# Optimization experiments

Measured on AMD Instinct MI355X. Metric: run time of the kernel, lower is better.

Reference implementation:

```python
import jax, jax.numpy as jnp
import numpy as np

TEMPERATURE = 0.07
BASE_TEMPERATURE = 0.07
EPS = 1e-10


def setup_inputs() -> dict:
    key = jax.random.key(0)
    k1, k2, k3 = jax.random.split(key, 3)
    bsz, n_views, d = 4096, 2, 256
    features = jax.random.normal(k1, (bsz, n_views, d), dtype=jnp.float32)
    # L2-normalize views as is standard for SupCon inputs (keeps logits sane)
    features = features / jnp.linalg.norm(features, axis=-1, keepdims=True)
    va_labels = jax.random.normal(k2, (bsz, 2), dtype=jnp.float32)
    batch_belong_diaID = jax.random.randint(k3, (bsz,), 0, 512, dtype=jnp.int64)
    return {
        "features": features,
        "va_labels": va_labels,
        "batch_belong_diaID": batch_belong_diaID,
        "thres_dict": 1,
    }


def reference(features, va_labels, batch_belong_diaID, thres_dict):
    bsz, n_views, d = features.shape
    dtype = features.dtype

    # --- vectorized mask construction (replaces O(bsz^2) python loops) ---
    eye = jnp.eye(bsz, dtype=bool)
    same_dia = batch_belong_diaID[:, None] == batch_belong_diaID[None, :]
    diff = va_labels[:, None, :] - va_labels[None, :, :]          # [bsz, bsz, 2]
    euclid = jnp.sqrt(jnp.sum(diff * diff, axis=-1))              # [bsz, bsz]
    close_va = euclid < thres_dict
    # final mask: diagonal | same dialogue | VA-close (off-diag terms; diag already 1)
    mask = (eye | same_dia | close_va).astype(dtype)
    mask = jax.lax.stop_gradient(mask)  # mask build is non-differentiable in torch too

    # --- contrastive loss (contrast_mode='one') ---
    # torch.cat(torch.unbind(features, 1), 0): view-major stacking
    contrast_feature = features.transpose(1, 0, 2).reshape(n_views * bsz, d)
    anchor_feature = features[:, 0]                               # anchor_count = 1

    logits = jnp.matmul(anchor_feature, contrast_feature.T) / TEMPERATURE  # [bsz, n_views*bsz]
    logits = logits - jax.lax.stop_gradient(jnp.max(logits, axis=1, keepdims=True))

    mask_t = jnp.tile(mask, (1, n_views))                          # [bsz, n_views*bsz]
    # logits_mask: zero out self-contrast (column i for anchor row i)
    idx = jnp.arange(bsz)
    logits_mask = jnp.ones((bsz, n_views * bsz), dtype=dtype).at[idx, idx].set(0.0)
    mask_t = mask_t * logits_mask

    exp_logits = jnp.exp(logits) * logits_mask
    log_prob = logits - jnp.log(jnp.sum(exp_logits, axis=1, keepdims=True) + EPS)

    mean_log_prob_pos = jnp.sum(mask_t * log_prob, axis=1) / (jnp.sum(mask_t, axis=1) + EPS)
    loss = jnp.mean(-mean_log_prob_pos)  # anchor_count=1 -> plain mean over bsz
    return loss
```

## Files before the change

### kernel.cpp

```cpp
#include <hip/hip_runtime.h>
#include <hip/hip_bf16.h>

#define BSZ   4096
#define NCON  8192
#define DFEAT 256
#define C2    20.60992914f
#define LN2   0.6931471806f

#define BJM 16
#define BI 128
#define NJT 8
#define JSTRIP_M (NJT * BJM)

typedef __attribute__((ext_vector_type(8))) short short8;
typedef __attribute__((ext_vector_type(4))) float f32x4;

__device__ __forceinline__ unsigned short f2bf(float f) {
    __hip_bfloat16 h = __float2bfloat16(f);
    return *reinterpret_cast<unsigned short*>(&h);
}

__device__ __forceinline__ void gload_lds16(const void* g, void* l) {
    __builtin_amdgcn_global_load_lds(
        (const __attribute__((address_space(1))) unsigned int*)g,
        (__attribute__((address_space(3))) unsigned int*)l,
        16, 0, 0);
}

__device__ __forceinline__ void gload_reg16(const void* p, short8& dst) {
    unsigned long long a = (unsigned long long)p;
    asm volatile("global_load_dwordx4 %0, %1, off"
                 : "=v"(dst) : "v"(a));
}


__global__ __launch_bounds__(256) void k_prep(const float* __restrict__ feat,
                                              unsigned short* __restrict__ con,
                                              float* __restrict__ acc) {
    int idx = blockIdx.x * 256 + threadIdx.x;
    int e = idx * 4;
    int j = e >> 8;
    int k = e & 255;
    int src = (j < BSZ) ? ((j * 2) * DFEAT + k)
                        : (((j - BSZ) * 2 + 1) * DFEAT + k);
    float4 f = *(const float4*)(feat + src);
    ushort4 o;
    o.x = f2bf(f.x); o.y = f2bf(f.y); o.z = f2bf(f.z); o.w = f2bf(f.w);
    *(ushort4*)(con + e) = o;
    if (idx < 3 * BSZ) acc[idx] = 0.0f;
}

__global__ __launch_bounds__(256) void k_main(const __hip_bfloat16* __restrict__ conp,
                                              const float* __restrict__ va,
                                              const int* __restrict__ dia,
                                              const int* __restrict__ thr_ptr,
                                              float* __restrict__ Srow,
                                              float* __restrict__ Arow,
                                              float* __restrict__ Brow) {
    __shared__ short lX[2][2][BJM * DFEAT];
    __shared__ float s_vjx[JSTRIP_M], s_vjy[JSTRIP_M];
    __shared__ int   s_dj[JSTRIP_M];

    const int tid  = threadIdx.x;
    const int lane = tid & 63;
    const int wv   = tid >> 6;
    const int l15  = lane & 15;
    const int hi   = lane >> 4;
    const int jmbase = blockIdx.x * JSTRIP_M;
    const int ibase  = blockIdx.y * BI + wv * 32;
    const short* cs = (const short*)conp;

    auto stageX = [&](int buf, int jt) {
        #pragma unroll
        for (int v = 0; v < 2; ++v) {
            #pragma unroll
            for (int q = 0; q < 2; ++q) {
                int e   = q * 2048 + tid * 8;
                int col = e & 63;
                int row = (e >> 6) & 15;
                int k2  = e >> 10;
                int scol = col ^ ((row & 7) << 3);
                gload_lds16(cs + (size_t)(jmbase + jt * BJM + row + v * BSZ) * DFEAT
                               + k2 * 64 + scol,
                            &lX[buf][v][e]);
            }
        }
    };

    stageX(0, 0);

    const short* yrow0 = cs + (size_t)(ibase + l15) * DFEAT + hi * 8;
    short8 y[2][8];
    #pragma unroll
    for (int n = 0; n < 2; ++n)
        #pragma unroll
        for (int s = 0; s < 8; ++s)
            gload_reg16(yrow0 + (size_t)n * 16 * DFEAT + s * 32, y[n][s]);

    if (tid < JSTRIP_M) {
        int jm = jmbase + tid;
        s_vjx[tid] = va[2 * jm]; s_vjy[tid] = va[2 * jm + 1]; s_dj[tid] = dia[jm];
    }

    int raw = *thr_ptr;
    float t_ = (raw > 0 && raw < 100000) ? (float)raw : __int_as_float(raw);
    float thres2 = t_ * t_;

    float vix[2], viy[2]; int di[2], ig[2];
    #pragma unroll
    for (int n = 0; n < 2; ++n) {
        ig[n] = ibase + n * 16 + l15;
        vix[n] = va[2 * ig[n]]; viy[n] = va[2 * ig[n] + 1]; di[n] = dia[ig[n]];
    }

    float sp[2] = {0.f, 0.f};
    float ap[2] = {0.f, 0.f};
    float bp[2] = {0.f, 0.f};

    __syncthreads();
    asm volatile("s_waitcnt vmcnt(0)" ::: "memory");
    __builtin_amdgcn_sched_barrier(0);

    for (int jt = 0; jt < NJT; ++jt) {
        const int cur = jt & 1;
        if (jt < NJT - 1) stageX(cur ^ 1, jt + 1);

        f32x4 acc[2][2];
        #pragma unroll
        for (int v = 0; v < 2; ++v)
            #pragma unroll
            for (int n = 0; n < 2; ++n)
                acc[v][n] = (f32x4){0.f, 0.f, 0.f, 0.f};

        __builtin_amdgcn_s_setprio(1);
        #pragma unroll
        for (int s = 0; s < 8; ++s) {
            const int base = (s >> 1) * 2048;
            const int colb = (s & 1) * 64 + hi * 16;
            const int row  = l15;
            const int off  = base + row * 128 + (colb ^ ((row & 7) << 4));
            short8 x0 = *(const short8*)((const char*)&lX[cur][0][0] + off);
            short8 x1 = *(const short8*)((const char*)&lX[cur][1][0] + off);
            #pragma unroll
            for (int n = 0; n < 2; ++n) {
                acc[0][n] = __builtin_amdgcn_mfma_f32_16x16x32_bf16(x0, y[n][s], acc[0][n], 0, 0, 0);
                acc[1][n] = __builtin_amdgcn_mfma_f32_16x16x32_bf16(x1, y[n][s], acc[1][n], 0, 0, 0);
            }
        }
        __builtin_amdgcn_s_setprio(0);

        const int jt0 = jt * BJM;
        #pragma unroll
        for (int r = 0; r < 4; ++r) {
            const int jl  = jt0 + hi * 4 + r;
            const int jmg = jmbase + jl;
            float vjx = s_vjx[jl], vjy = s_vjy[jl];
            int dj = s_dj[jl];
            #pragma unroll
            for (int n = 0; n < 2; ++n) {
                float l0 = __builtin_fmaf(acc[0][n][r], C2, -C2);
                float l1 = __builtin_fmaf(acc[1][n][r], C2, -C2);
                float dx = vix[n] - vjx, dy = viy[n] - vjy;
                bool diag = (ig[n] == jmg);
                bool mk = (di[n] == dj) | (dx * dx + dy * dy < thres2);
                float e0 = diag ? 0.0f : exp2f(l0);
                float e1 = exp2f(l1);
                sp[n] += e0 + e1;
                float mm = mk ? 1.0f : 0.0f;
                ap[n] = __builtin_fmaf(mm, l0 + l1, ap[n]);
                bp[n] += mm;
            }
        }
        __syncthreads();
    }

    #pragma unroll
    for (int n = 0; n < 2; ++n) {
        float s = sp[n], a = ap[n], b = bp[n];
        s += __shfl_xor(s, 16, 64);  a += __shfl_xor(a, 16, 64);  b += __shfl_xor(b, 16, 64);
        s += __shfl_xor(s, 32, 64);  a += __shfl_xor(a, 32, 64);  b += __shfl_xor(b, 32, 64);
        if (hi == 0) {
            atomicAdd(&Srow[ig[n]], s);
            atomicAdd(&Arow[ig[n]], a * LN2);
            atomicAdd(&Brow[ig[n]], b);
        }
    }
}

__global__ __launch_bounds__(256) void k_final(const float* __restrict__ S,
                                               const float* __restrict__ A,
                                               const float* __restrict__ B,
                                               float* __restrict__ out) {
    __shared__ float red[256];
    float sum = 0.f;
    for (int i = threadIdx.x; i < BSZ; i += 256) {
        float b = 2.0f * B[i] - 1.0f;
        float v = (A[i] - b * logf(S[i] + 1e-10f)) / (b + 1e-10f);
        sum += -v;
    }
    red[threadIdx.x] = sum;
    __syncthreads();
    for (int s = 128; s > 0; s >>= 1) {
        if (threadIdx.x < s) red[threadIdx.x] += red[threadIdx.x + s];
        __syncthreads();
    }
    if (threadIdx.x == 0) out[0] = red[0] / (float)BSZ;
}

extern "C" void kernel_launch(void* const* d_in, const int* in_sizes, int n_in,
                              void* d_out, int out_size, void* d_ws, size_t ws_size,
                              hipStream_t stream) {
    const float* feat = (const float*)d_in[0];
    const float* va   = (const float*)d_in[1];
    const int*   dia  = (const int*)d_in[2];
    const int*   thr  = (const int*)d_in[3];

    unsigned short* con = (unsigned short*)d_ws;
    float* acc = (float*)((char*)d_ws + (size_t)NCON * DFEAT * 2);
    float* out = (float*)d_out;

    k_prep<<<(NCON * DFEAT / 4 + 255) / 256, 256, 0, stream>>>(feat, con, acc);

    dim3 grid(BSZ / JSTRIP_M, BSZ / BI);
    k_main<<<grid, 256, 0, stream>>>((const __hip_bfloat16*)con, va, dia, thr,
                                     acc, acc + BSZ, acc + 2 * BSZ);

    k_final<<<1, 256, 0, stream>>>(acc, acc + BSZ, acc + 2 * BSZ, out);
}
```

Measured before the change: 51.06 us.

## Double j-tile height to 32 rows with precomputed staging pointers and packed metadata

Doubles the per-iteration j tile from 16 to 32 rows, so each wave now runs 8 MFMAs per k-step over two 16-row sub-tiles and each strip covers 256 columns. This halves the grid's x dimension and the number of barriers per unit of work. Global-to-LDS staging addresses are now precomputed once and advanced by pointer increments. Per-column va/dialog metadata is packed into one float4 LDS array so it needs a single load. The trade-off is twice the LDS for the double buffer, about 64KB, which may lower occupancy, plus more accumulator registers and fewer blocks in flight.

```diff
diff --git a/kernel.cpp b/kernel.cpp
--- a/kernel.cpp
+++ b/kernel.cpp
@@ -7,7 +7,7 @@
 #define C2    20.60992914f
 #define LN2   0.6931471806f
 
-#define BJM 16
+#define BJM 32
 #define BI 128
 #define NJT 8
 #define JSTRIP_M (NJT * BJM)
@@ -58,8 +58,7 @@
                                               float* __restrict__ Arow,
                                               float* __restrict__ Brow) {
     __shared__ short lX[2][2][BJM * DFEAT];
-    __shared__ float s_vjx[JSTRIP_M], s_vjy[JSTRIP_M];
-    __shared__ int   s_dj[JSTRIP_M];
+    __shared__ float4 s_meta[JSTRIP_M];
 
     const int tid  = threadIdx.x;
     const int lane = tid & 63;
@@ -70,24 +69,30 @@
     const int ibase  = blockIdx.y * BI + wv * 32;
     const short* cs = (const short*)conp;
 
-    auto stageX = [&](int buf, int jt) {
-        #pragma unroll
-        for (int v = 0; v < 2; ++v) {
-            #pragma unroll
-            for (int q = 0; q < 2; ++q) {
-                int e   = q * 2048 + tid * 8;
-                int col = e & 63;
-                int row = (e >> 6) & 15;
-                int k2  = e >> 10;
-                int scol = col ^ ((row & 7) << 3);
-                gload_lds16(cs + (size_t)(jmbase + jt * BJM + row + v * BSZ) * DFEAT
-                               + k2 * 64 + scol,
-                            &lX[buf][v][e]);
+    const short* pg[2][4];
+    #pragma unroll
+    for (int v = 0; v < 2; ++v)
+        #pragma unroll
+        for (int q = 0; q < 4; ++q) {
+            int e   = q * 2048 + tid * 8;
+            int col = e & 63;
+            int row = (e >> 6) & 31;
+            int k2  = e >> 11;
+            int scol = col ^ ((row & 7) << 3);
+            pg[v][q] = cs + (size_t)(jmbase + row + v * BSZ) * DFEAT + k2 * 64 + scol;
+        }
+
+    auto stageX = [&](int buf) {
+        #pragma unroll
+        for (int v = 0; v < 2; ++v)
+            #pragma unroll
+            for (int q = 0; q < 4; ++q) {
+                gload_lds16(pg[v][q], &lX[buf][v][q * 2048 + tid * 8]);
+                pg[v][q] += BJM * DFEAT;
             }
-        }
     };
 
-    stageX(0, 0);
+    stageX(0);
 
     const short* yrow0 = cs + (size_t)(ibase + l15) * DFEAT + hi * 8;
     short8 y[2][8];
@@ -97,9 +102,10 @@
         for (int s = 0; s < 8; ++s)
             gload_reg16(yrow0 + (size_t)n * 16 * DFEAT + s * 32, y[n][s]);
 
-    if (tid < JSTRIP_M) {
+    {
         int jm = jmbase + tid;
-        s_vjx[tid] = va[2 * jm]; s_vjy[tid] = va[2 * jm + 1]; s_dj[tid] = dia[jm];
+        s_meta[tid] = make_float4(va[2 * jm], va[2 * jm + 1],
+                                  __int_as_float(dia[jm]), 0.0f);
     }
 
     int raw = *thr_ptr;
@@ -123,54 +129,66 @@
 
     for (int jt = 0; jt < NJT; ++jt) {
         const int cur = jt & 1;
-        if (jt < NJT - 1) stageX(cur ^ 1, jt + 1);
-
-        f32x4 acc[2][2];
+        if (jt < NJT - 1) stageX(cur ^ 1);
+
+        f32x4 acc[2][2][2];
         #pragma unroll
         for (int v = 0; v < 2; ++v)
             #pragma unroll
-            for (int n = 0; n < 2; ++n)
-                acc[v][n] = (f32x4){0.f, 0.f, 0.f, 0.f};
+            for (int m = 0; m < 2; ++m)
+                #pragma unroll
+                for (int n = 0; n < 2; ++n)
+                    acc[v][m][n] = (f32x4){0.f, 0.f, 0.f, 0.f};
 
         __builtin_amdgcn_s_setprio(1);
         #pragma unroll
         for (int s = 0; s < 8; ++s) {
-            const int base = (s >> 1) * 2048;
+            const int base = (s >> 1) * 4096;
             const int colb = (s & 1) * 64 + hi * 16;
-            const int row  = l15;
-            const int off  = base + row * 128 + (colb ^ ((row & 7) << 4));
-            short8 x0 = *(const short8*)((const char*)&lX[cur][0][0] + off);
-            short8 x1 = *(const short8*)((const char*)&lX[cur][1][0] + off);
-            #pragma unroll
-            for (int n = 0; n < 2; ++n) {
-                acc[0][n] = __builtin_amdgcn_mfma_f32_16x16x32_bf16(x0, y[n][s], acc[0][n], 0, 0, 0);
-                acc[1][n] = __builtin_amdgcn_mfma_f32_16x16x32_bf16(x1, y[n][s], acc[1][n], 0, 0, 0);
-            }
+            short8 xf[2][2];
+            #pragma unroll
+            for (int v = 0; v < 2; ++v)
+                #pragma unroll
+                for (int m = 0; m < 2; ++m) {
+                    int row = m * 16 + l15;
+                    xf[v][m] = *(const short8*)((const char*)&lX[cur][v][0]
+                                 + base + row * 128 + (colb ^ ((row & 7) << 4)));
+                }
+            #pragma unroll
+            for (int v = 0; v < 2; ++v)
+                #pragma unroll
+                for (int m = 0; m < 2; ++m)
+                    #pragma unroll
+                    for (int n = 0; n < 2; ++n)
+                        acc[v][m][n] = __builtin_amdgcn_mfma_f32_16x16x32_bf16(
+                            xf[v][m], y[n][s], acc[v][m][n], 0, 0, 0);
         }
         __builtin_amdgcn_s_setprio(0);
 
         const int jt0 = jt * BJM;
         #pragma unroll
-        for (int r = 0; r < 4; ++r) {
-            const int jl  = jt0 + hi * 4 + r;
-            const int jmg = jmbase + jl;
-            float vjx = s_vjx[jl], vjy = s_vjy[jl];
-            int dj = s_dj[jl];
-            #pragma unroll
-            for (int n = 0; n < 2; ++n) {
-                float l0 = __builtin_fmaf(acc[0][n][r], C2, -C2);
-                float l1 = __builtin_fmaf(acc[1][n][r], C2, -C2);
-                float dx = vix[n] - vjx, dy = viy[n] - vjy;
-                bool diag = (ig[n] == jmg);
-                bool mk = (di[n] == dj) | (dx * dx + dy * dy < thres2);
-                float e0 = diag ? 0.0f : exp2f(l0);
-                float e1 = exp2f(l1);
-                sp[n] += e0 + e1;
-                float mm = mk ? 1.0f : 0.0f;
-                ap[n] = __builtin_fmaf(mm, l0 + l1, ap[n]);
-                bp[n] += mm;
+        for (int m = 0; m < 2; ++m)
+            #pragma unroll
+            for (int r = 0; r < 4; ++r) {
+                const int jl  = jt0 + m * 16 + hi * 4 + r;
+                const int jmg = jmbase + jl;
+                float4 md = s_meta[jl];
+                int dj = __float_as_int(md.z);
+                #pragma unroll
+                for (int n = 0; n < 2; ++n) {
+                    float l0 = __builtin_fmaf(acc[0][m][n][r], C2, -C2);
+                    float l1 = __builtin_fmaf(acc[1][m][n][r], C2, -C2);
+                    float dx = vix[n] - md.x, dy = viy[n] - md.y;
+                    bool diag = (ig[n] == jmg);
+                    bool mk = (di[n] == dj) | (dx * dx + dy * dy < thres2);
+                    float e0 = diag ? 0.0f : exp2f(l0);
+                    float e1 = exp2f(l1);
+                    sp[n] += e0 + e1;
+                    float mm = mk ? 1.0f : 0.0f;
+                    ap[n] = __builtin_fmaf(mm, l0 + l1, ap[n]);
+                    bp[n] += mm;
+                }
             }
-        }
         __syncthreads();
     }
 
```

Result: slower. 57.84 us (+13.3%).

## Triple-buffer LDS staging with vmcnt-based waits and longer j-strips

Applied to the files above, without the earlier changes.

Moves the X tile staging from a double buffer to a three-stage LDS ring, prefetching two tiles ahead. Each iteration uses a partial vmcnt wait followed by a single barrier, replacing the trailing __syncthreads. It also doubles the j-strip length per block (NJT 8→16), which halves the grid's column dimension, removes the s_setprio hints, and sets launch bounds to three waves per SIMD. The diagonal mask handling moves into the main kernel so the final kernel uses B directly. The larger LDS footprint and fewer blocks may reduce occupancy or parallelism in exchange for deeper load overlap.

```diff
diff --git a/kernel.cpp b/kernel.cpp
--- a/kernel.cpp
+++ b/kernel.cpp
@@ -9,7 +9,7 @@
 
 #define BJM 16
 #define BI 128
-#define NJT 8
+#define NJT 16
 #define JSTRIP_M (NJT * BJM)
 
 typedef __attribute__((ext_vector_type(8))) short short8;
@@ -50,14 +50,14 @@
     if (idx < 3 * BSZ) acc[idx] = 0.0f;
 }
 
-__global__ __launch_bounds__(256) void k_main(const __hip_bfloat16* __restrict__ conp,
-                                              const float* __restrict__ va,
-                                              const int* __restrict__ dia,
-                                              const int* __restrict__ thr_ptr,
-                                              float* __restrict__ Srow,
-                                              float* __restrict__ Arow,
-                                              float* __restrict__ Brow) {
-    __shared__ short lX[2][2][BJM * DFEAT];
+__global__ __launch_bounds__(256, 3) void k_main(const __hip_bfloat16* __restrict__ conp,
+                                                 const float* __restrict__ va,
+                                                 const int* __restrict__ dia,
+                                                 const int* __restrict__ thr_ptr,
+                                                 float* __restrict__ Srow,
+                                                 float* __restrict__ Arow,
+                                                 float* __restrict__ Brow) {
+    __shared__ short lX[3][2][BJM * DFEAT];
     __shared__ float s_vjx[JSTRIP_M], s_vjy[JSTRIP_M];
     __shared__ int   s_dj[JSTRIP_M];
 
@@ -88,7 +88,7 @@
     };
 
     stageX(0, 0);
-
+    __builtin_amdgcn_sched_barrier(0);
     const short* yrow0 = cs + (size_t)(ibase + l15) * DFEAT + hi * 8;
     short8 y[2][8];
     #pragma unroll
@@ -96,8 +96,11 @@
         #pragma unroll
         for (int s = 0; s < 8; ++s)
             gload_reg16(yrow0 + (size_t)n * 16 * DFEAT + s * 32, y[n][s]);
-
-    if (tid < JSTRIP_M) {
+    __builtin_amdgcn_sched_barrier(0);
+    stageX(1, 1);
+    __builtin_amdgcn_sched_barrier(0);
+
+    {
         int jm = jmbase + tid;
         s_vjx[tid] = va[2 * jm]; s_vjy[tid] = va[2 * jm + 1]; s_dj[tid] = dia[jm];
     }
@@ -117,14 +120,18 @@
     float ap[2] = {0.f, 0.f};
     float bp[2] = {0.f, 0.f};
 
-    __syncthreads();
-    asm volatile("s_waitcnt vmcnt(0)" ::: "memory");
-    __builtin_amdgcn_sched_barrier(0);
-
-    for (int jt = 0; jt < NJT; ++jt) {
-        const int cur = jt & 1;
-        if (jt < NJT - 1) stageX(cur ^ 1, jt + 1);
-
+    asm volatile("s_waitcnt lgkmcnt(0)" ::: "memory");
+
+    #pragma unroll 1
+    for (int t = 0; t < NJT; ++t) {
+        if (t < NJT - 1) asm volatile("s_waitcnt vmcnt(4)" ::: "memory");
+        else             asm volatile("s_waitcnt vmcnt(0)" ::: "memory");
+        __builtin_amdgcn_sched_barrier(0);
+        __builtin_amdgcn_s_barrier();
+
+        if (t < NJT - 2) stageX((t + 2) % 3, t + 2);
+
+        const int cur = t % 3;
         f32x4 acc[2][2];
         #pragma unroll
         for (int v = 0; v < 2; ++v)
@@ -132,7 +139,6 @@
             for (int n = 0; n < 2; ++n)
                 acc[v][n] = (f32x4){0.f, 0.f, 0.f, 0.f};
 
-        __builtin_amdgcn_s_setprio(1);
         #pragma unroll
         for (int s = 0; s < 8; ++s) {
             const int base = (s >> 1) * 2048;
@@ -147,9 +153,8 @@
                 acc[1][n] = __builtin_amdgcn_mfma_f32_16x16x32_bf16(x1, y[n][s], acc[1][n], 0, 0, 0);
             }
         }
-        __builtin_amdgcn_s_setprio(0);
-
-        const int jt0 = jt * BJM;
+
+        const int jt0 = t * BJM;
         #pragma unroll
         for (int r = 0; r < 4; ++r) {
             const int jl  = jt0 + hi * 4 + r;
@@ -162,16 +167,17 @@
                 float l1 = __builtin_fmaf(acc[1][n][r], C2, -C2);
                 float dx = vix[n] - vjx, dy = viy[n] - vjy;
                 bool diag = (ig[n] == jmg);
-                bool mk = (di[n] == dj) | (dx * dx + dy * dy < thres2);
+                bool mk = diag | (di[n] == dj) | (dx * dx + dy * dy < thres2);
                 float e0 = diag ? 0.0f : exp2f(l0);
                 float e1 = exp2f(l1);
                 sp[n] += e0 + e1;
-                float mm = mk ? 1.0f : 0.0f;
-                ap[n] = __builtin_fmaf(mm, l0 + l1, ap[n]);
-                bp[n] += mm;
+                float m1f = mk ? 1.0f : 0.0f;
+                float m0f = (mk & !diag) ? 1.0f : 0.0f;
+                ap[n] = __builtin_fmaf(m0f, l0, ap[n]);
+                ap[n] = __builtin_fmaf(m1f, l1, ap[n]);
+                bp[n] += m0f + m1f;
             }
         }
-        __syncthreads();
     }
 
     #pragma unroll
@@ -194,7 +200,7 @@
     __shared__ float red[256];
     float sum = 0.f;
     for (int i = threadIdx.x; i < BSZ; i += 256) {
-        float b = 2.0f * B[i] - 1.0f;
+        float b = B[i];
         float v = (A[i] - b * logf(S[i] + 1e-10f)) / (b + 1e-10f);
         sum += -v;
     }
```

Result: faster. 48.62 us (-4.8%).
